# Performance work log

Hardware: AMD Instinct MI355X
Metric: run time of the kernel (lower is better)

The kernel has to match this reference:

```python
import jax, jax.numpy as jnp
import numpy as np

B, S, D, H, HD, RN, FF, WIN = 2, 2048, 2048, 16, 128, 32, 4096, 256
NEG = float(np.finfo(np.float16).min)  # torch.finfo(torch.float16).min
EPS = 1e-5
SCALE = 1.0 / float(np.sqrt(HD))


def _ln(x, w, b):
    m = jnp.mean(x, -1, keepdims=True)
    v = jnp.mean((x - m) ** 2, -1, keepdims=True)
    return (x - m) * jax.lax.rsqrt(v + EPS) * w + b


def _rms(x, w):
    return x * jax.lax.rsqrt(jnp.mean(x * x, -1, keepdims=True) + EPS) * w


def _rope_half(x, fc):
    # x: (B,S,H,RN); fc: (S,RN//2,2). Half-split input pairs, interleaved output
    # (faithful to apply_rotary_emb mode='half' + flatten(3)).
    half = x.shape[-1] // 2
    x0, x1 = x[..., :half], x[..., half:]
    c = fc[None, :, None, :, 0]
    s = fc[None, :, None, :, 1]
    out = jnp.stack([x0 * c - x1 * s, x1 * c + x0 * s], -1)  # (B,S,H,half,2)
    return out.reshape(x.shape)


def setup_inputs() -> dict:
    key = jax.random.key(0)
    ks = jax.random.split(key, 8)
    w = lambda k, shape: 0.02 * jax.random.normal(k, shape, jnp.float32)
    x = jax.random.normal(ks[0], (B, S, D), jnp.float32)
    # real rotary table: angles t * 10000^(-2i/RN), stored as (cos, sin)
    inv = 1.0 / (10000.0 ** (np.arange(0, RN, 2) / RN))  # (RN//2,)
    ang = np.arange(S)[:, None] * inv[None, :]           # (S, RN//2)
    freqs_cis = jnp.asarray(np.stack([np.cos(ang), np.sin(ang)], -1), jnp.float32)
    # sliding-window causal mask, window = 256
    i = np.arange(S)
    m = (i[None, :] <= i[:, None]) & ((i[:, None] - i[None, :]) < WIN)
    mask = jnp.asarray(m)[None, None]  # (1,1,S,S) bool
    return {
        "x": x, "freqs_cis": freqs_cis, "mask": mask,
        "wqkv_w": w(ks[1], (D, 3 * D)), "wqkv_b": jnp.zeros((3 * D,), jnp.float32),
        "wo_w": w(ks[2], (D, D)), "wo_b": jnp.zeros((D,), jnp.float32),
        "qn_w": jnp.ones((HD,), jnp.float32), "kn_w": jnp.ones((HD,), jnp.float32),
        "attn_ln_w": jnp.ones((D,), jnp.float32), "attn_ln_b": jnp.zeros((D,), jnp.float32),
        "ffn_ln_w": jnp.ones((D,), jnp.float32), "ffn_ln_b": jnp.zeros((D,), jnp.float32),
        "w1_w": w(ks[3], (D, FF)), "w1_b": jnp.zeros((FF,), jnp.float32),
        "w2_w": w(ks[4], (FF, D)), "w2_b": jnp.zeros((D,), jnp.float32),
    }


def reference(x, freqs_cis, mask, wqkv_w, wqkv_b, wo_w, wo_b, qn_w, kn_w,
              attn_ln_w, attn_ln_b, ffn_ln_w, ffn_ln_b, w1_w, w1_b, w2_w, w2_b):
    bsz, seqlen, _ = x.shape
    nx = _ln(x, attn_ln_w, attn_ln_b)
    qkv = nx @ wqkv_w + wqkv_b                       # (B,S,3D)
    q, k, v = jnp.split(qkv, [D, 2 * D], axis=-1)
    q = q.reshape(bsz, seqlen, H, HD)
    k = k.reshape(bsz, seqlen, H, HD)
    v = v.reshape(bsz, seqlen, H, HD)
    # QK-RMSNorm
    q, k = _rms(q, qn_w), _rms(k, kn_w)
    # partial rotary (first RN dims)
    q = jnp.concatenate([_rope_half(q[..., :RN], freqs_cis), q[..., RN:]], -1)
    k = jnp.concatenate([_rope_half(k[..., :RN], freqs_cis), k[..., RN:]], -1)
    # attention with windowed mask
    logits = jnp.einsum("bqhd,bkhd->bhqk", q, k) * SCALE
    logits = jnp.where(mask, logits, NEG)
    probs = jax.nn.softmax(logits, axis=-1)
    y = jnp.einsum("bhqk,bkhd->bqhd", probs, v).reshape(bsz, seqlen, D)
    attn_out = y @ wo_w + wo_b
    h = x + attn_out
    # parallel residual: FFN reads ffn_norm(res) with res = x
    f = _ln(x, ffn_ln_w, ffn_ln_b)
    ffn = jax.nn.gelu(f @ w1_w + w1_b, approximate=False) @ w2_w + w2_b
    return h + ffn
```

## Files before the change

kernel.cpp:

```cpp
#include <hip/hip_runtime.h>


typedef unsigned short u16;
typedef unsigned int   u32;
typedef __bf16 bf16x8 __attribute__((ext_vector_type(8)));
typedef float  f32x4  __attribute__((ext_vector_type(4)));

#define B_    2
#define S_    2048
#define D_    2048
#define H_    16
#define HD_   128
#define FF_   4096
#define WIN_  256
#define EPS_  1e-5f
#define SCALE_ 0.08838834764831845f

__device__ __forceinline__ float b2f(u16 u) {
    return __uint_as_float(((u32)u) << 16);
}
__device__ __forceinline__ u16 f2b(float f) {
    u32 u = __float_as_uint(f);
    u32 r = (u + 0x7fffu + ((u >> 16) & 1u)) >> 16;
    return (u16)r;
}
__device__ __forceinline__ float wave_sum(float v) {
#pragma unroll
    for (int o = 32; o > 0; o >>= 1) v += __shfl_xor(v, o);
    return v;
}

__global__ __launch_bounds__(256) void transpose_k(const float* __restrict__ in,
                                                   u16* __restrict__ out,
                                                   int R, int C) {
    __shared__ float tile[32][33];
    int tx = threadIdx.x & 31, ty = threadIdx.x >> 5;
    int c0 = blockIdx.x * 32, r0 = blockIdx.y * 32;
#pragma unroll
    for (int i = 0; i < 32; i += 8)
        tile[ty + i][tx] = in[(size_t)(r0 + ty + i) * C + c0 + tx];
    __syncthreads();
#pragma unroll
    for (int i = 0; i < 32; i += 8)
        out[(size_t)(c0 + ty + i) * R + r0 + tx] = f2b(tile[tx][ty + i]);
}

__global__ __launch_bounds__(256) void ln_dual(const float* __restrict__ x,
        const float* __restrict__ aw, const float* __restrict__ ab,
        const float* __restrict__ fw, const float* __restrict__ fb,
        u16* __restrict__ nx, u16* __restrict__ f) {
    int row = blockIdx.x;
    const float* xr = x + (size_t)row * D_;
    int base = threadIdx.x * 8;
    float4 xa = *(const float4*)&xr[base];
    float4 xb = *(const float4*)&xr[base + 4];
    float xv[8] = {xa.x, xa.y, xa.z, xa.w, xb.x, xb.y, xb.z, xb.w};
    float s = 0.f, s2 = 0.f;
#pragma unroll
    for (int i = 0; i < 8; ++i) { s += xv[i]; s2 += xv[i] * xv[i]; }
    s = wave_sum(s); s2 = wave_sum(s2);
    __shared__ float r1[4], r2[4];
    int w = threadIdx.x >> 6;
    if ((threadIdx.x & 63) == 0) { r1[w] = s; r2[w] = s2; }
    __syncthreads();
    float ts  = r1[0] + r1[1] + r1[2] + r1[3];
    float ts2 = r2[0] + r2[1] + r2[2] + r2[3];
    float mean = ts * (1.f / D_);
    float var  = ts2 * (1.f / D_) - mean * mean;
    float inv  = rsqrtf(var + EPS_);
    float4 wa0 = *(const float4*)&aw[base], wa1 = *(const float4*)&aw[base + 4];
    float4 ba0 = *(const float4*)&ab[base], ba1 = *(const float4*)&ab[base + 4];
    float4 wf0 = *(const float4*)&fw[base], wf1 = *(const float4*)&fw[base + 4];
    float4 bf0 = *(const float4*)&fb[base], bf1 = *(const float4*)&fb[base + 4];
    float wav[8] = {wa0.x, wa0.y, wa0.z, wa0.w, wa1.x, wa1.y, wa1.z, wa1.w};
    float bav[8] = {ba0.x, ba0.y, ba0.z, ba0.w, ba1.x, ba1.y, ba1.z, ba1.w};
    float wfv[8] = {wf0.x, wf0.y, wf0.z, wf0.w, wf1.x, wf1.y, wf1.z, wf1.w};
    float bfv[8] = {bf0.x, bf0.y, bf0.z, bf0.w, bf1.x, bf1.y, bf1.z, bf1.w};
    union { uint4 v; u16 s[8]; } o1, o2;
#pragma unroll
    for (int i = 0; i < 8; ++i) {
        float t = (xv[i] - mean) * inv;
        o1.s[i] = f2b(t * wav[i] + bav[i]);
        o2.s[i] = f2b(t * wfv[i] + bfv[i]);
    }
    *(uint4*)&nx[(size_t)row * D_ + base] = o1.v;
    *(uint4*)&f [(size_t)row * D_ + base] = o2.v;
}

template <int EPI>
__global__ __launch_bounds__(256, 2) void gemm_bt(
        const u16* __restrict__ A, const u16* __restrict__ BT,
        const float* __restrict__ bias, const float* __restrict__ res,
        void* __restrict__ Cv, int M, int N, int K) {
    __shared__ __align__(16) u16 As[128][40];
    __shared__ __align__(16) u16 Bs[128][40];
    int m0 = blockIdx.y * 128, n0 = blockIdx.x * 128;
    int w = threadIdx.x >> 6, lane = threadIdx.x & 63;
    int wm = (w >> 1) * 64, wn = (w & 1) * 64;
    int row16 = lane & 15, quad = lane >> 4;
    int tr = threadIdx.x >> 2, tc = (threadIdx.x & 3) * 8;
    f32x4 acc[4][4] = {};
    for (int k0 = 0; k0 < K; k0 += 32) {
        __syncthreads();
        *(uint4*)&As[tr][tc]      = *(const uint4*)&A [(size_t)(m0 + tr)      * K + k0 + tc];
        *(uint4*)&As[tr + 64][tc] = *(const uint4*)&A [(size_t)(m0 + tr + 64) * K + k0 + tc];
        *(uint4*)&Bs[tr][tc]      = *(const uint4*)&BT[(size_t)(n0 + tr)      * K + k0 + tc];
        *(uint4*)&Bs[tr + 64][tc] = *(const uint4*)&BT[(size_t)(n0 + tr + 64) * K + k0 + tc];
        __syncthreads();
        bf16x8 af[4], bfr[4];
#pragma unroll
        for (int i = 0; i < 4; ++i) {
            af[i]  = *(const bf16x8*)&As[wm + i * 16 + row16][quad * 8];
            bfr[i] = *(const bf16x8*)&Bs[wn + i * 16 + row16][quad * 8];
        }
#pragma unroll
        for (int mi = 0; mi < 4; ++mi)
#pragma unroll
            for (int ni = 0; ni < 4; ++ni)
                acc[mi][ni] = __builtin_amdgcn_mfma_f32_16x16x32_bf16(
                        af[mi], bfr[ni], acc[mi][ni], 0, 0, 0);
    }
#pragma unroll
    for (int mi = 0; mi < 4; ++mi) {
#pragma unroll
        for (int ni = 0; ni < 4; ++ni) {
            int gcol = n0 + wn + ni * 16 + row16;
            float bv = bias[gcol];
#pragma unroll
            for (int i = 0; i < 4; ++i) {
                int grow = m0 + wm + mi * 16 + quad * 4 + i;
                float vv = acc[mi][ni][i] + bv;
                if (EPI == 1) {
                    vv += res[(size_t)grow * N + gcol];
                    ((float*)Cv)[(size_t)grow * N + gcol] = vv;
                } else {
                    if (EPI == 2)
                        vv = vv * 0.5f * (1.0f + erff(vv * 0.70710678118654752f));
                    ((u16*)Cv)[(size_t)grow * N + gcol] = f2b(vv);
                }
            }
        }
    }
}

__global__ __launch_bounds__(256) void qk_rope(const u16* __restrict__ qkv,
        const float* __restrict__ qn_w, const float* __restrict__ kn_w,
        const float* __restrict__ freqs,
        u16* __restrict__ q, u16* __restrict__ k) {
    int w = threadIdx.x >> 6, lane = threadIdx.x & 63;
    int unit = blockIdx.x * 4 + w;
    int h = unit & (H_ - 1);
    int s = (unit >> 4) & (S_ - 1);
    int b = unit >> 15;
    size_t inbase  = (size_t)(b * S_ + s) * (3 * D_) + h * HD_;
    size_t outbase = ((size_t)((b * H_ + h) * S_) + s) * HD_;
    int t = (lane & 31) >> 1;
    float c  = freqs[(s * 16 + t) * 2];
    float sn = freqs[(s * 16 + t) * 2 + 1];
#pragma unroll
    for (int part = 0; part < 2; ++part) {
        const float* nw = part ? kn_w : qn_w;
        size_t ib = inbase + (size_t)part * D_;
        float a0 = b2f(qkv[ib + lane]);
        float a1 = b2f(qkv[ib + 64 + lane]);
        float ss = wave_sum(a0 * a0 + a1 * a1);
        float inv = rsqrtf(ss * (1.f / HD_) + EPS_);
        float n0 = a0 * inv * nw[lane];
        float n1 = a1 * inv * nw[64 + lane];
        float x0 = __shfl(n0, t);
        float x1 = __shfl(n0, t + 16);
        float roped = (lane & 1) ? (x1 * c + x0 * sn) : (x0 * c - x1 * sn);
        float out0 = (lane < 32) ? roped : n0;
        u16* dst = part ? k : q;
        dst[outbase + lane]      = f2b(out0);
        dst[outbase + 64 + lane] = f2b(n1);
    }
}

__global__ __launch_bounds__(256) void v_transpose(const u32* __restrict__ qkv32,
                                                   u32* __restrict__ vt32) {
    __shared__ u32 tile[64][17];
    int bh = blockIdx.z; int b = bh >> 4, h = bh & 15;
    int s0 = blockIdx.x * 64, d0 = blockIdx.y * 32;
    int tid = threadIdx.x;
    int rr = tid >> 4, cc = tid & 15;
#pragma unroll
    for (int i = 0; i < 4; ++i) {
        int s = s0 + rr + i * 16;
        tile[rr + i * 16][cc] =
            qkv32[(size_t)(b * S_ + s) * (3 * D_ / 2) + (2 * D_ + h * HD_ + d0) / 2 + cc];
    }
    __syncthreads();
    int dr = tid & 31, sc = tid >> 5;
#pragma unroll
    for (int i = 0; i < 4; ++i) {
        int s2 = sc + i * 8;
        u32 w0 = tile[2 * s2][dr >> 1];
        u32 w1 = tile[2 * s2 + 1][dr >> 1];
        u32 h0 = (dr & 1) ? (w0 >> 16) : (w0 & 0xffffu);
        u32 h1 = (dr & 1) ? (w1 >> 16) : (w1 & 0xffffu);
        vt32[((size_t)bh * HD_ + d0 + dr) * (S_ / 2) + (s0 >> 1) + s2] = h0 | (h1 << 16);
    }
}

__global__ __launch_bounds__(256) void attn_mfma(
        const u16* __restrict__ q, const u16* __restrict__ k,
        const u16* __restrict__ vt, u16* __restrict__ y) {
    __shared__ __align__(16) u16 Ks [64][136];
    __shared__ __align__(16) u16 Vts[128][72];
    __shared__ __align__(16) u16 Ps [4][16][72];
    int g  = blockIdx.x & (S_ / 64 - 1);
    int bh = blockIdx.x >> 5;
    int qbase = g * 64;
    size_t kvbase = (size_t)bh * S_ * HD_;
    size_t vtbase = (size_t)bh * HD_ * S_;
    int w = threadIdx.x >> 6, lane = threadIdx.x & 63;
    int col16 = lane & 15, quad = lane >> 4;
    int q0w = qbase + w * 16;
    bf16x8 af[4];
#pragma unroll
    for (int kb = 0; kb < 4; ++kb)
        af[kb] = *(const bf16x8*)&q[kvbase + (size_t)(q0w + col16) * HD_ + kb * 32 + quad * 8];
    f32x4 oacc[8] = {};
    float mrow[4], lrow[4];
#pragma unroll
    for (int i = 0; i < 4; ++i) { mrow[i] = -1e38f; lrow[i] = 0.f; }
    int t0 = g >= 4 ? g - 4 : 0;
    int tid = threadIdx.x;
    int kr = tid >> 2, kc = (tid & 3) * 32;
    int vr = tid >> 1, vc = (tid & 1) * 32;
    for (int t = t0; t <= g; ++t) {
        __syncthreads();
        {
            const u16* kg = &k[kvbase + (size_t)(t * 64 + kr) * HD_ + kc];
#pragma unroll
            for (int i = 0; i < 4; ++i)
                *(uint4*)&Ks[kr][kc + i * 8] = *(const uint4*)&kg[i * 8];
            const u16* vg = &vt[vtbase + (size_t)vr * S_ + t * 64 + vc];
#pragma unroll
            for (int i = 0; i < 4; ++i)
                *(uint4*)&Vts[vr][vc + i * 8] = *(const uint4*)&vg[i * 8];
        }
        __syncthreads();
        f32x4 sacc[4] = {};
#pragma unroll
        for (int ks = 0; ks < 4; ++ks)
#pragma unroll
            for (int kb = 0; kb < 4; ++kb) {
                bf16x8 bf = *(const bf16x8*)&Ks[ks * 16 + col16][kb * 32 + quad * 8];
                sacc[ks] = __builtin_amdgcn_mfma_f32_16x16x32_bf16(af[kb], bf, sacc[ks], 0, 0, 0);
            }
        float pm[4][4];
        float tmax[4] = {-3e38f, -3e38f, -3e38f, -3e38f};
#pragma unroll
        for (int ks = 0; ks < 4; ++ks) {
            int jg = t * 64 + ks * 16 + col16;
#pragma unroll
            for (int i = 0; i < 4; ++i) {
                int qi = q0w + quad * 4 + i;
                bool valid = (jg <= qi) && (qi - jg < WIN_);
                float sv = valid ? sacc[ks][i] * SCALE_ : -3e38f;
                pm[ks][i] = sv;
                tmax[i] = fmaxf(tmax[i], sv);
            }
        }
#pragma unroll
        for (int off = 8; off >= 1; off >>= 1)
#pragma unroll
            for (int i = 0; i < 4; ++i)
                tmax[i] = fmaxf(tmax[i], __shfl_xor(tmax[i], off));
        float alpha[4], psum[4];
#pragma unroll
        for (int i = 0; i < 4; ++i) {
            float mnew = fmaxf(mrow[i], tmax[i]);
            alpha[i] = __expf(mrow[i] - mnew);
            mrow[i] = mnew;
            psum[i] = 0.f;
        }
#pragma unroll
        for (int ks = 0; ks < 4; ++ks)
#pragma unroll
            for (int i = 0; i < 4; ++i) {
                float p = __expf(pm[ks][i] - mrow[i]);
                psum[i] += p;
                Ps[w][quad * 4 + i][ks * 16 + col16] = f2b(p);
            }
#pragma unroll
        for (int off = 8; off >= 1; off >>= 1)
#pragma unroll
            for (int i = 0; i < 4; ++i)
                psum[i] += __shfl_xor(psum[i], off);
#pragma unroll
        for (int i = 0; i < 4; ++i)
            lrow[i] = lrow[i] * alpha[i] + psum[i];
#pragma unroll
        for (int ns = 0; ns < 8; ++ns)
#pragma unroll
            for (int i = 0; i < 4; ++i)
                oacc[ns][i] *= alpha[i];
#pragma unroll
        for (int c = 0; c < 2; ++c) {
            bf16x8 pf = *(const bf16x8*)&Ps[w][col16][c * 32 + quad * 8];
#pragma unroll
            for (int ns = 0; ns < 8; ++ns) {
                bf16x8 vf = *(const bf16x8*)&Vts[ns * 16 + col16][c * 32 + quad * 8];
                oacc[ns] = __builtin_amdgcn_mfma_f32_16x16x32_bf16(pf, vf, oacc[ns], 0, 0, 0);
            }
        }
    }
    int b = bh >> 4, hh = bh & 15;
#pragma unroll
    for (int i = 0; i < 4; ++i) {
        int qi = q0w + quad * 4 + i;
        float invl = 1.f / lrow[i];
        size_t ob = (size_t)(b * S_ + qi) * D_ + hh * HD_;
#pragma unroll
        for (int ns = 0; ns < 8; ++ns)
            y[ob + ns * 16 + col16] = f2b(oacc[ns][i] * invl);
    }
}

extern "C" void kernel_launch(void* const* d_in, const int* in_sizes, int n_in,
                              void* d_out, int out_size, void* d_ws, size_t ws_size,
                              hipStream_t stream) {
    const float* x      = (const float*)d_in[0];
    const float* freqs  = (const float*)d_in[1];
    const float* wqkv_w = (const float*)d_in[3];
    const float* wqkv_b = (const float*)d_in[4];
    const float* wo_w   = (const float*)d_in[5];
    const float* wo_b   = (const float*)d_in[6];
    const float* qn_w   = (const float*)d_in[7];
    const float* kn_w   = (const float*)d_in[8];
    const float* aln_w  = (const float*)d_in[9];
    const float* aln_b  = (const float*)d_in[10];
    const float* fln_w  = (const float*)d_in[11];
    const float* fln_b  = (const float*)d_in[12];
    const float* w1_w   = (const float*)d_in[13];
    const float* w1_b   = (const float*)d_in[14];
    const float* w2_w   = (const float*)d_in[15];
    const float* w2_b   = (const float*)d_in[16];
    float* out = (float*)d_out;

    char* ws = (char*)d_ws;
    size_t off = 0;
    auto alloc = [&](size_t bytes) { char* p = ws + off; off += (bytes + 255) & ~(size_t)255; return (u16*)p; };
    const size_t E = sizeof(u16);
    u16* wt_qkv = alloc((size_t)D_ * 3 * D_ * E);
    u16* wt_wo  = alloc((size_t)D_ * D_ * E);
    u16* wt_w1  = alloc((size_t)D_ * FF_ * E);
    u16* wt_w2  = alloc((size_t)FF_ * D_ * E);
    u16* nx     = alloc((size_t)B_ * S_ * D_ * E);
    u16* f      = alloc((size_t)B_ * S_ * D_ * E);
    u16* qkv    = alloc((size_t)B_ * S_ * 3 * D_ * E);
    u16* qb     = alloc((size_t)B_ * S_ * D_ * E);
    u16* kb     = alloc((size_t)B_ * S_ * D_ * E);
    u16* vtb    = alloc((size_t)B_ * S_ * D_ * E);
    u16* y    = nx;
    u16* tmid = qkv;
    float* h  = out;

    if (off > ws_size) return;

    const int M = B_ * S_;

    transpose_k<<<dim3(3 * D_ / 32, D_ / 32), 256, 0, stream>>>(wqkv_w, wt_qkv, D_, 3 * D_);
    transpose_k<<<dim3(D_ / 32, D_ / 32),     256, 0, stream>>>(wo_w,   wt_wo,  D_, D_);
    transpose_k<<<dim3(FF_ / 32, D_ / 32),    256, 0, stream>>>(w1_w,   wt_w1,  D_, FF_);
    transpose_k<<<dim3(D_ / 32, FF_ / 32),    256, 0, stream>>>(w2_w,   wt_w2,  FF_, D_);

    ln_dual<<<M, 256, 0, stream>>>(x, aln_w, aln_b, fln_w, fln_b, nx, f);

    gemm_bt<0><<<dim3(3 * D_ / 128, M / 128), 256, 0, stream>>>(nx, wt_qkv, wqkv_b, nullptr, qkv, M, 3 * D_, D_);

    qk_rope<<<B_ * S_ * H_ / 4, 256, 0, stream>>>(qkv, qn_w, kn_w, freqs, qb, kb);
    v_transpose<<<dim3(S_ / 64, HD_ / 32, B_ * H_), 256, 0, stream>>>((const u32*)qkv, (u32*)vtb);

    attn_mfma<<<B_ * H_ * (S_ / 64), 256, 0, stream>>>(qb, kb, vtb, y);

    gemm_bt<2><<<dim3(FF_ / 128, M / 128), 256, 0, stream>>>(f, wt_w1, w1_b, nullptr, tmid, M, FF_, D_);

    gemm_bt<1><<<dim3(D_ / 128, M / 128), 256, 0, stream>>>(y, wt_wo, wo_b, x, h, M, D_, D_);

    gemm_bt<1><<<dim3(D_ / 128, M / 128), 256, 0, stream>>>(tmid, wt_w2, w2_b, h, out, M, D_, FF_);
}
```

Baseline: 714.5 us.

## Use direct global-to-LDS loads in GEMM, widen transposes and rope accesses

```diff
diff --git a/kernel.cpp b/kernel.cpp
--- a/kernel.cpp
+++ b/kernel.cpp
@@ -5,6 +5,8 @@
 typedef unsigned int   u32;
 typedef __bf16 bf16x8 __attribute__((ext_vector_type(8)));
 typedef float  f32x4  __attribute__((ext_vector_type(4)));
+typedef __attribute__((address_space(3))) u32 as3_u32;
+typedef __attribute__((address_space(1))) u32 as1_u32;
 
 #define B_    2
 #define S_    2048
@@ -29,20 +31,35 @@
     for (int o = 32; o > 0; o >>= 1) v += __shfl_xor(v, o);
     return v;
 }
+__device__ __forceinline__ void gld_lds16(const u16* g, u16* l) {
+    __builtin_amdgcn_global_load_lds((const as1_u32*)g, (as3_u32*)l, 16, 0, 0);
+}
 
 __global__ __launch_bounds__(256) void transpose_k(const float* __restrict__ in,
                                                    u16* __restrict__ out,
                                                    int R, int C) {
-    __shared__ float tile[32][33];
-    int tx = threadIdx.x & 31, ty = threadIdx.x >> 5;
-    int c0 = blockIdx.x * 32, r0 = blockIdx.y * 32;
-#pragma unroll
-    for (int i = 0; i < 32; i += 8)
-        tile[ty + i][tx] = in[(size_t)(r0 + ty + i) * C + c0 + tx];
+    __shared__ float tile[64][65];
+    int t = threadIdx.x;
+    int r0 = blockIdx.y * 64, c0 = blockIdx.x * 64;
+    int rr = t >> 2;
+    int cb = (t & 3) * 16;
+    const float* src = &in[(size_t)(r0 + rr) * C + c0 + cb];
+#pragma unroll
+    for (int j = 0; j < 16; j += 4) {
+        float4 v = *(const float4*)&src[j];
+        tile[rr][cb + j]     = v.x; tile[rr][cb + j + 1] = v.y;
+        tile[rr][cb + j + 2] = v.z; tile[rr][cb + j + 3] = v.w;
+    }
     __syncthreads();
-#pragma unroll
-    for (int i = 0; i < 32; i += 8)
-        out[(size_t)(c0 + ty + i) * R + r0 + tx] = f2b(tile[tx][ty + i]);
+    int wq = t & 31;
+    int ch = t >> 5;
+#pragma unroll
+    for (int i = 0; i < 8; ++i) {
+        int c = ch * 8 + i;
+        u32 lo = (u32)f2b(tile[2 * wq][c]);
+        u32 hi = (u32)f2b(tile[2 * wq + 1][c]);
+        ((u32*)out)[(((size_t)(c0 + c) * R) >> 1) + (r0 >> 1) + wq] = lo | (hi << 16);
+    }
 }
 
 __global__ __launch_bounds__(256) void ln_dual(const float* __restrict__ x,
@@ -92,20 +109,21 @@
         const u16* __restrict__ A, const u16* __restrict__ BT,
         const float* __restrict__ bias, const float* __restrict__ res,
         void* __restrict__ Cv, int M, int N, int K) {
-    __shared__ __align__(16) u16 As[128][40];
-    __shared__ __align__(16) u16 Bs[128][40];
+    __shared__ __align__(16) u16 As[128][32];
+    __shared__ __align__(16) u16 Bs[128][32];
     int m0 = blockIdx.y * 128, n0 = blockIdx.x * 128;
     int w = threadIdx.x >> 6, lane = threadIdx.x & 63;
     int wm = (w >> 1) * 64, wn = (w & 1) * 64;
     int row16 = lane & 15, quad = lane >> 4;
-    int tr = threadIdx.x >> 2, tc = (threadIdx.x & 3) * 8;
+    int lr = lane >> 2;
+    int lc = (lane & 3) * 8;
     f32x4 acc[4][4] = {};
     for (int k0 = 0; k0 < K; k0 += 32) {
         __syncthreads();
-        *(uint4*)&As[tr][tc]      = *(const uint4*)&A [(size_t)(m0 + tr)      * K + k0 + tc];
-        *(uint4*)&As[tr + 64][tc] = *(const uint4*)&A [(size_t)(m0 + tr + 64) * K + k0 + tc];
-        *(uint4*)&Bs[tr][tc]      = *(const uint4*)&BT[(size_t)(n0 + tr)      * K + k0 + tc];
-        *(uint4*)&Bs[tr + 64][tc] = *(const uint4*)&BT[(size_t)(n0 + tr + 64) * K + k0 + tc];
+        gld_lds16(&A [(size_t)(m0 +      w * 16 + lr) * K + k0 + lc], &As[     w * 16][0]);
+        gld_lds16(&A [(size_t)(m0 + 64 + w * 16 + lr) * K + k0 + lc], &As[64 + w * 16][0]);
+        gld_lds16(&BT[(size_t)(n0 +      w * 16 + lr) * K + k0 + lc], &Bs[     w * 16][0]);
+        gld_lds16(&BT[(size_t)(n0 + 64 + w * 16 + lr) * K + k0 + lc], &Bs[64 + w * 16][0]);
         __syncthreads();
         bf16x8 af[4], bfr[4];
 #pragma unroll
@@ -143,37 +161,43 @@
     }
 }
 
-__global__ __launch_bounds__(256) void qk_rope(const u16* __restrict__ qkv,
+__global__ __launch_bounds__(256) void qk_rope(const u32* __restrict__ qkv32,
         const float* __restrict__ qn_w, const float* __restrict__ kn_w,
         const float* __restrict__ freqs,
-        u16* __restrict__ q, u16* __restrict__ k) {
+        u32* __restrict__ q32, u32* __restrict__ k32) {
     int w = threadIdx.x >> 6, lane = threadIdx.x & 63;
     int unit = blockIdx.x * 4 + w;
     int h = unit & (H_ - 1);
     int s = (unit >> 4) & (S_ - 1);
     int b = unit >> 15;
-    size_t inbase  = (size_t)(b * S_ + s) * (3 * D_) + h * HD_;
-    size_t outbase = ((size_t)((b * H_ + h) * S_) + s) * HD_;
-    int t = (lane & 31) >> 1;
-    float c  = freqs[(s * 16 + t) * 2];
-    float sn = freqs[(s * 16 + t) * 2 + 1];
+    size_t inbase  = (size_t)(b * S_ + s) * (3 * D_ / 2) + h * (HD_ / 2);
+    size_t outbase = ((size_t)((b * H_ + h) * S_) + s) * (HD_ / 2);
+    float fc = 0.f, fs = 0.f;
+    if (lane < 16) {
+        fc = freqs[(s * 16 + lane) * 2];
+        fs = freqs[(s * 16 + lane) * 2 + 1];
+    }
 #pragma unroll
     for (int part = 0; part < 2; ++part) {
         const float* nw = part ? kn_w : qn_w;
-        size_t ib = inbase + (size_t)part * D_;
-        float a0 = b2f(qkv[ib + lane]);
-        float a1 = b2f(qkv[ib + 64 + lane]);
+        u32 wv = qkv32[inbase + part * (D_ / 2) + lane];
+        float a0 = b2f((u16)(wv & 0xffffu));
+        float a1 = b2f((u16)(wv >> 16));
         float ss = wave_sum(a0 * a0 + a1 * a1);
         float inv = rsqrtf(ss * (1.f / HD_) + EPS_);
-        float n0 = a0 * inv * nw[lane];
-        float n1 = a1 * inv * nw[64 + lane];
-        float x0 = __shfl(n0, t);
-        float x1 = __shfl(n0, t + 16);
-        float roped = (lane & 1) ? (x1 * c + x0 * sn) : (x0 * c - x1 * sn);
-        float out0 = (lane < 32) ? roped : n0;
-        u16* dst = part ? k : q;
-        dst[outbase + lane]      = f2b(out0);
-        dst[outbase + 64 + lane] = f2b(n1);
+        float2 nwp = *(const float2*)&nw[2 * lane];
+        float n0 = a0 * inv * nwp.x;
+        float n1 = a1 * inv * nwp.y;
+        float e0 = __shfl(n0, lane >> 1), e1 = __shfl(n1, lane >> 1);
+        float o0 = __shfl(n0, 8 + (lane >> 1)), o1 = __shfl(n1, 8 + (lane >> 1));
+        float x0 = (lane & 1) ? e1 : e0;
+        float x1 = (lane & 1) ? o1 : o0;
+        float rv0 = x0 * fc - x1 * fs;
+        float rv1 = x1 * fc + x0 * fs;
+        float w0 = (lane < 16) ? rv0 : n0;
+        float w1 = (lane < 16) ? rv1 : n1;
+        u32* dst = part ? k32 : q32;
+        dst[outbase + lane] = (u32)f2b(w0) | ((u32)f2b(w1) << 16);
     }
 }
 
@@ -363,16 +387,16 @@
 
     const int M = B_ * S_;
 
-    transpose_k<<<dim3(3 * D_ / 32, D_ / 32), 256, 0, stream>>>(wqkv_w, wt_qkv, D_, 3 * D_);
-    transpose_k<<<dim3(D_ / 32, D_ / 32),     256, 0, stream>>>(wo_w,   wt_wo,  D_, D_);
-    transpose_k<<<dim3(FF_ / 32, D_ / 32),    256, 0, stream>>>(w1_w,   wt_w1,  D_, FF_);
-    transpose_k<<<dim3(D_ / 32, FF_ / 32),    256, 0, stream>>>(w2_w,   wt_w2,  FF_, D_);
+    transpose_k<<<dim3(3 * D_ / 64, D_ / 64), 256, 0, stream>>>(wqkv_w, wt_qkv, D_, 3 * D_);
+    transpose_k<<<dim3(D_ / 64, D_ / 64),     256, 0, stream>>>(wo_w,   wt_wo,  D_, D_);
+    transpose_k<<<dim3(FF_ / 64, D_ / 64),    256, 0, stream>>>(w1_w,   wt_w1,  D_, FF_);
+    transpose_k<<<dim3(D_ / 64, FF_ / 64),    256, 0, stream>>>(w2_w,   wt_w2,  FF_, D_);
 
     ln_dual<<<M, 256, 0, stream>>>(x, aln_w, aln_b, fln_w, fln_b, nx, f);
 
     gemm_bt<0><<<dim3(3 * D_ / 128, M / 128), 256, 0, stream>>>(nx, wt_qkv, wqkv_b, nullptr, qkv, M, 3 * D_, D_);
 
-    qk_rope<<<B_ * S_ * H_ / 4, 256, 0, stream>>>(qkv, qn_w, kn_w, freqs, qb, kb);
+    qk_rope<<<B_ * S_ * H_ / 4, 256, 0, stream>>>((const u32*)qkv, qn_w, kn_w, freqs, (u32*)qb, (u32*)kb);
     v_transpose<<<dim3(S_ / 64, HD_ / 32, B_ * H_), 256, 0, stream>>>((const u32*)qkv, (u32*)vtb);
 
     attn_mfma<<<B_ * H_ * (S_ / 64), 256, 0, stream>>>(qb, kb, vtb, y);
```

Result: faster. 696.5 us (-2.5%).
